# Kernel optimization log

Measured on AMD Instinct MI355X. Metric: run time of the kernel, lower is better.

Reference implementation:

```python
import jax, jax.numpy as jnp
import numpy as np


def setup_inputs() -> dict:
    key = jax.random.key(0)
    k1, k2, k3 = jax.random.split(key, 3)
    N, H, K, E = 16384, 1024, 8, 64
    x = jax.random.normal(k1, (N, H), dtype=jnp.float32)
    expert_idx = jax.random.randint(k2, (N, K), 0, E, dtype=jnp.int32)
    scale = jax.random.uniform(k3, (N,), dtype=jnp.float32)
    return {"x": x, "expert_idx": expert_idx, "scale": scale, "expert_num": E}


def reference(x, expert_idx, scale, expert_num):
    # MoE init routing v2, dropless (drop_pad_mode=0), no quant (quant_mode=0),
    # expert_tokens_num_type=0 -> cumulative counts over [0, expert_num).
    N, K = expert_idx.shape
    NK = N * K
    flat_expert = expert_idx.reshape(NK)
    # stable sort by expert id: all (token, k) slots for expert 0 first, etc.
    sort_idx = jnp.argsort(flat_expert, stable=True)          # [N*K]
    token_rows = sort_idx // K                                 # source token per expanded row
    expanded_x = x[token_rows]                                 # [N*K, H] gather
    # inverse permutation: expanded_row_idx[n*K + k] = position in expanded_x
    expanded_row_idx = jnp.zeros((NK,), dtype=jnp.int32).at[sort_idx].set(
        jnp.arange(NK, dtype=jnp.int32))
    # per-expert token counts -> cumulative sum
    counts = jax.ops.segment_sum(jnp.ones((NK,), dtype=jnp.int64),
                                 flat_expert, num_segments=expert_num)
    expert_token_cumsum = jnp.cumsum(counts)                   # [expert_num]
    expanded_scale = scale[token_rows]                         # [N*K]
    return (expanded_x, expanded_row_idx, expert_token_cumsum, expanded_scale)
```

## Files before the change

kernel.cpp:

```cpp
#include <hip/hip_runtime.h>

#define TPB 256

typedef float f32x4 __attribute__((ext_vector_type(4)));

__global__ void k_hist(const int* __restrict__ eidx, int* __restrict__ blockHist,
                       int NK, int E) {
    __shared__ int hist[256];
    int tid = threadIdx.x;
    for (int e = tid; e < E; e += TPB) hist[e] = 0;
    __syncthreads();
    int j = blockIdx.x * TPB + tid;
    if (j < NK) atomicAdd(&hist[eidx[j]], 1);
    __syncthreads();
    for (int e = tid; e < E; e += TPB)
        blockHist[(size_t)blockIdx.x * E + e] = hist[e];
}

__global__ void k_scan_blocks(int* __restrict__ blockHist, int* __restrict__ counts,
                              int numBlocks, int E) {
    __shared__ int s[TPB];
    int e = blockIdx.x;
    int tid = threadIdx.x;
    int per = (numBlocks + TPB - 1) / TPB;
    int start = tid * per;
    int end = start + per; if (end > numBlocks) end = numBlocks;
    int sum = 0;
    for (int b = start; b < end; ++b) sum += blockHist[(size_t)b * E + e];
    s[tid] = sum;
    __syncthreads();
    for (int off = 1; off < TPB; off <<= 1) {
        int t = (tid >= off) ? s[tid - off] : 0;
        __syncthreads();
        s[tid] += t;
        __syncthreads();
    }
    int run = (tid == 0) ? 0 : s[tid - 1];
    if (tid == TPB - 1) counts[e] = s[tid];
    for (int b = start; b < end; ++b) {
        size_t idx = (size_t)b * E + e;
        int v = blockHist[idx];
        blockHist[idx] = run;
        run += v;
    }
}

__global__ void __launch_bounds__(TPB) k_pos(
        const int* __restrict__ eidx, const float* __restrict__ scale,
        const int* __restrict__ blockHist, const int* __restrict__ counts,
        float* __restrict__ row_idx_out, float* __restrict__ scale_out,
        float* __restrict__ cumsum_out, int* __restrict__ dstPos,
        int NK, int E, int K) {
    __shared__ int whist[4 * 256];
    __shared__ int wbase[4 * 256];
    __shared__ int cnt_sh[256];
    __shared__ int inc_sh[256];
    int tid  = threadIdx.x;
    int j    = blockIdx.x * TPB + tid;
    int wv   = tid >> 6;
    int lane = tid & 63;

    for (int i = tid; i < 4 * E; i += TPB) whist[i] = 0;
    if (tid < E) { int c = counts[tid]; cnt_sh[tid] = c; inc_sh[tid] = c; }
    __syncthreads();

    for (int off = 1; off < E; off <<= 1) {
        int v = 0;
        if (tid < E && tid >= off) v = inc_sh[tid - off];
        __syncthreads();
        if (tid < E) inc_sh[tid] += v;
        __syncthreads();
    }
    if (blockIdx.x == 0 && tid < E) cumsum_out[tid] = (float)inc_sh[tid];

    bool valid = (j < NK);
    int e = valid ? eidx[j] : 0;

    unsigned long long mask = __ballot(valid);
    #pragma unroll
    for (int b = 0; b < 8; ++b) {
        unsigned long long bal = __ballot((e >> b) & 1);
        mask &= ((e >> b) & 1) ? bal : ~bal;
    }
    unsigned long long lt = (1ULL << lane) - 1ULL;
    int rank_in_wave = (int)__popcll(mask & lt);
    bool leader = valid && ((mask & lt) == 0);
    if (leader) whist[wv * E + e] = (int)__popcll(mask);
    __syncthreads();

    for (int ee = tid; ee < E; ee += TPB) {
        int base = 0;
        #pragma unroll
        for (int w = 0; w < 4; ++w) {
            wbase[w * E + ee] = base;
            base += whist[w * E + ee];
        }
    }
    __syncthreads();

    if (valid) {
        int off_e = inc_sh[e] - cnt_sh[e];
        int pos = off_e + blockHist[(size_t)blockIdx.x * E + e]
                + wbase[wv * E + e] + rank_in_wave;
        row_idx_out[j] = (float)pos;
        dstPos[j] = pos;
        scale_out[pos] = scale[j / K];
    }
}

__global__ void k_scatter(const float* __restrict__ x, const int* __restrict__ dstPos,
                          float* __restrict__ out, int H, int K, int N) {
    __shared__ int pos_s[32];
    int n4 = H >> 2;
    int tok = blockIdx.x;
    if (tok >= N) return;
    const f32x4* xs = (const f32x4*)(x + (size_t)tok * H);
    int tid = threadIdx.x;
    f32x4 v0;
    bool have0 = (tid < n4);
    if (have0) v0 = xs[tid];
    if (tid < K) pos_s[tid] = dstPos[tok * K + tid];
    __syncthreads();
    for (int t = tid; t < n4; t += blockDim.x) {
        f32x4 v = (t == tid) ? v0 : xs[t];
        #pragma unroll
        for (int k = 0; k < 8; ++k) {
            if (k < K) {
                f32x4* od = (f32x4*)(out + (size_t)pos_s[k] * H);
                __builtin_nontemporal_store(v, od + t);
            }
        }
    }
}

extern "C" void kernel_launch(void* const* d_in, const int* in_sizes, int n_in,
                              void* d_out, int out_size, void* d_ws, size_t ws_size,
                              hipStream_t stream) {
    const float* x     = (const float*)d_in[0];
    const int*   eidx  = (const int*)d_in[1];
    const float* scale = (const float*)d_in[2];

    const int N  = in_sizes[2];
    const int H  = in_sizes[0] / N;
    const int K  = in_sizes[1] / N;
    const int NK = N * K;
    const int E  = out_size - (int)((long long)NK * H) - 2 * NK;

    const int numBlocks = (NK + TPB - 1) / TPB;

    float* out_x     = (float*)d_out;
    float* out_rowix = out_x + (size_t)NK * H;
    float* out_cum   = out_rowix + NK;
    float* out_scale = out_cum + E;

    int* blockHist = (int*)d_ws;
    int* counts    = blockHist + (size_t)numBlocks * E;
    int* dstPos    = counts + E;

    k_hist<<<numBlocks, TPB, 0, stream>>>(eidx, blockHist, NK, E);
    k_scan_blocks<<<E, TPB, 0, stream>>>(blockHist, counts, numBlocks, E);
    k_pos<<<numBlocks, TPB, 0, stream>>>(eidx, scale, blockHist, counts,
                                         out_rowix, out_scale, out_cum, dstPos,
                                         NK, E, K);
    k_scatter<<<N, TPB, 0, stream>>>(x, dstPos, out_x, H, K, N);
}
```

Before: 121.3 us.

## Fuse position computation into per-token scatter kernel

Merges the position/rank kernel into the scatter kernel so that each token block recomputes the ranks of its 256-slot chunk in shared memory and then writes row indices, scales and the gathered rows directly. This removes one kernel launch and the global dstPos write and read round trip. In exchange, the histogram and rank work is repeated redundantly by every token block in a chunk.

```diff
diff --git a/kernel.cpp b/kernel.cpp
--- a/kernel.cpp
+++ b/kernel.cpp
@@ -45,20 +45,31 @@
     }
 }
 
-__global__ void __launch_bounds__(TPB) k_pos(
+__global__ void __launch_bounds__(TPB) k_pos_scatter(
         const int* __restrict__ eidx, const float* __restrict__ scale,
         const int* __restrict__ blockHist, const int* __restrict__ counts,
+        const float* __restrict__ x,
         float* __restrict__ row_idx_out, float* __restrict__ scale_out,
-        float* __restrict__ cumsum_out, int* __restrict__ dstPos,
-        int NK, int E, int K) {
+        float* __restrict__ cumsum_out, float* __restrict__ out_x,
+        int NK, int E, int K, int H) {
     __shared__ int whist[4 * 256];
     __shared__ int wbase[4 * 256];
     __shared__ int cnt_sh[256];
     __shared__ int inc_sh[256];
+    __shared__ int pos_sh[TPB];
     int tid  = threadIdx.x;
-    int j    = blockIdx.x * TPB + tid;
+    int tok  = blockIdx.x;
+    int tpc  = TPB / K;
+    int chunk = tok / tpc;
+    int j    = chunk * TPB + tid;
     int wv   = tid >> 6;
     int lane = tid & 63;
+
+    const f32x4* xs = (const f32x4*)(x + (size_t)tok * H);
+    int n4 = H >> 2;
+    f32x4 v0;
+    bool have0 = (tid < n4);
+    if (have0) v0 = xs[tid];
 
     for (int i = tid; i < 4 * E; i += TPB) whist[i] = 0;
     if (tid < E) { int c = counts[tid]; cnt_sh[tid] = c; inc_sh[tid] = c; }
@@ -100,34 +111,30 @@
 
     if (valid) {
         int off_e = inc_sh[e] - cnt_sh[e];
-        int pos = off_e + blockHist[(size_t)blockIdx.x * E + e]
-                + wbase[wv * E + e] + rank_in_wave;
-        row_idx_out[j] = (float)pos;
-        dstPos[j] = pos;
-        scale_out[pos] = scale[j / K];
+        pos_sh[tid] = off_e + blockHist[(size_t)chunk * E + e]
+                    + wbase[wv * E + e] + rank_in_wave;
     }
-}
+    __syncthreads();
 
-__global__ void k_scatter(const float* __restrict__ x, const int* __restrict__ dstPos,
-                          float* __restrict__ out, int H, int K, int N) {
-    __shared__ int pos_s[32];
-    int n4 = H >> 2;
-    int tok = blockIdx.x;
-    if (tok >= N) return;
-    const f32x4* xs = (const f32x4*)(x + (size_t)tok * H);
-    int tid = threadIdx.x;
-    f32x4 v0;
-    bool have0 = (tid < n4);
-    if (have0) v0 = xs[tid];
-    if (tid < K) pos_s[tid] = dstPos[tok * K + tid];
-    __syncthreads();
-    for (int t = tid; t < n4; t += blockDim.x) {
-        f32x4 v = (t == tid) ? v0 : xs[t];
-        #pragma unroll
-        for (int k = 0; k < 8; ++k) {
-            if (k < K) {
-                f32x4* od = (f32x4*)(out + (size_t)pos_s[k] * H);
-                __builtin_nontemporal_store(v, od + t);
+    int s0 = (tok - chunk * tpc) * K;
+    if (tid < K) {
+        int jj = chunk * TPB + s0 + tid;
+        if (jj < NK) {
+            int p = pos_sh[s0 + tid];
+            row_idx_out[jj] = (float)p;
+            scale_out[p] = scale[tok];
+        }
+    }
+
+    if ((size_t)tok * K < (size_t)NK) {
+        for (int t = tid; t < n4; t += TPB) {
+            f32x4 v = (t == tid) ? v0 : xs[t];
+            #pragma unroll
+            for (int k = 0; k < 8; ++k) {
+                if (k < K) {
+                    f32x4* od = (f32x4*)(out_x + (size_t)pos_sh[s0 + k] * H);
+                    __builtin_nontemporal_store(v, od + t);
+                }
             }
         }
     }
@@ -155,12 +162,10 @@
 
     int* blockHist = (int*)d_ws;
     int* counts    = blockHist + (size_t)numBlocks * E;
-    int* dstPos    = counts + E;
 
     k_hist<<<numBlocks, TPB, 0, stream>>>(eidx, blockHist, NK, E);
     k_scan_blocks<<<E, TPB, 0, stream>>>(blockHist, counts, numBlocks, E);
-    k_pos<<<numBlocks, TPB, 0, stream>>>(eidx, scale, blockHist, counts,
-                                         out_rowix, out_scale, out_cum, dstPos,
-                                         NK, E, K);
-    k_scatter<<<N, TPB, 0, stream>>>(x, dstPos, out_x, H, K, N);
+    k_pos_scatter<<<N, TPB, 0, stream>>>(eidx, scale, blockHist, counts, x,
+                                         out_rowix, out_scale, out_cum, out_x,
+                                         NK, E, K, H);
 }
```

New measurement: 118.5 us. 1.02x faster.
